# Performance work log

Hardware: AMD Instinct MI355X
Metric: run time of the kernel (lower is better)

## Reference

```python
import jax, jax.numpy as jnp
import numpy as np

NUM_HEADS = 12
WS = 8
ROPE_BASE = 100.0  # croco/dust3r RoPE2D default frequency base


def _rope1d(t, p, inv_freq):
    # t: [Bw, h, N, d], p: [Bw, N], inv_freq: [d/2]
    freqs = p[..., None] * inv_freq                      # [Bw, N, d/2]
    emb = jnp.concatenate([freqs, freqs], axis=-1)       # [Bw, N, d]
    cos = jnp.cos(emb)[:, None, :, :]
    sin = jnp.sin(emb)[:, None, :, :]
    t1, t2 = jnp.split(t, 2, axis=-1)
    rot = jnp.concatenate([-t2, t1], axis=-1)            # rotate_half
    return t * cos + rot * sin


def _rope2d(tokens, pos):
    # tokens: [Bw, h, N, D], pos: [Bw, N, 2] (y, x). First D/2 dims use y, last D/2 use x.
    D = tokens.shape[-1]
    d = D // 2
    inv_freq = 1.0 / (ROPE_BASE ** (jnp.arange(0, d, 2, dtype=jnp.float32) / d))
    ty, tx = jnp.split(tokens, 2, axis=-1)
    return jnp.concatenate([_rope1d(ty, pos[..., 0], inv_freq),
                            _rope1d(tx, pos[..., 1], inv_freq)], axis=-1)


def setup_inputs() -> dict:
    B, H, W, C = 16, 64, 64, 768
    key = jax.random.key(0)
    ks = jax.random.split(key, 7)
    x_img = jax.random.normal(ks[0], (B, H * W, C), dtype=jnp.float32)
    yy, xx = jnp.meshgrid(jnp.arange(H), jnp.arange(W), indexing='ij')
    pos = jnp.stack([yy, xx], axis=-1).reshape(1, H * W, 2).astype(jnp.float32)
    pos2d_img = jnp.broadcast_to(pos, (B, H * W, 2))
    unseen = jax.random.normal(ks[1], (B, C), dtype=jnp.float32)
    sc = C ** -0.5
    qkv_w = jax.random.normal(ks[2], (3 * C, C), dtype=jnp.float32) * sc
    qkv_b = jax.random.normal(ks[3], (3 * C,), dtype=jnp.float32) * 0.02
    proj_w = jax.random.normal(ks[4], (C, C), dtype=jnp.float32) * sc
    proj_b = jax.random.normal(ks[5], (C,), dtype=jnp.float32) * 0.02
    return {'x_img': x_img, 'pos2d_img': pos2d_img, 'unseen': unseen,
            'qkv_w': qkv_w, 'qkv_b': qkv_b, 'proj_w': proj_w, 'proj_b': proj_b,
            'H': H, 'W': W}


def reference(x_img, pos2d_img, unseen, qkv_w, qkv_b, proj_w, proj_b, H, W):
    B, HW, C = x_img.shape
    hd = C // NUM_HEADS
    scale = hd ** -0.5
    nWh, nWw = H // WS, W // WS
    Bwin, Nwin = B * nWh * nWw, WS * WS

    # window partition
    xw = x_img.reshape(B, nWh, WS, nWw, WS, C).transpose(0, 1, 3, 2, 4, 5).reshape(Bwin, Nwin, C)
    pw = pos2d_img.reshape(B, nWh, WS, nWw, WS, 2).transpose(0, 1, 3, 2, 4, 5).reshape(Bwin, Nwin, 2)

    # append unseen token (shared across windows of an image)
    u = jnp.broadcast_to(unseen[:, None, None, :], (B, nWh * nWw, 1, C)).reshape(Bwin, 1, C)
    xw = jnp.concatenate([xw, u], axis=1)                # [Bwin, Nwin+1, C]

    qkv = xw @ qkv_w.T + qkv_b                           # [Bwin, N, 3C]
    qkv = qkv.reshape(Bwin, Nwin + 1, 3, NUM_HEADS, hd)
    q = qkv[:, :, 0].transpose(0, 2, 1, 3)               # [Bwin, h, N, hd]
    k = qkv[:, :, 1].transpose(0, 2, 1, 3)
    v = qkv[:, :, 2].transpose(0, 2, 1, 3)

    # RoPE2D on image tokens only; unseen token gets no RoPE
    q = jnp.concatenate([_rope2d(q[:, :, :Nwin], pw), q[:, :, Nwin:]], axis=2)
    k = jnp.concatenate([_rope2d(k[:, :, :Nwin], pw), k[:, :, Nwin:]], axis=2)

    attn = jax.nn.softmax(jnp.einsum('bhqd,bhkd->bhqk', q, k) * scale, axis=-1)
    out = jnp.einsum('bhqk,bhkd->bhqd', attn, v)
    out = out.transpose(0, 2, 1, 3).reshape(Bwin, Nwin + 1, C)
    out = out @ proj_w.T + proj_b

    # window merge
    out_img = out[:, :Nwin].reshape(B, nWh, nWw, WS, WS, C).transpose(0, 1, 3, 2, 4, 5).reshape(B, HW, C)
    out_unseen = out[:, Nwin].reshape(B, nWh * nWw, C).mean(axis=1)  # [B, C]
    return out_img, out_unseen
```

## Files before the change

kernel.cpp:

```cpp
#include <hip/hip_runtime.h>
#include <cstdint>
#include <cstddef>

typedef __attribute__((ext_vector_type(8)))  __bf16 bf16x8;
typedef __attribute__((ext_vector_type(4)))  float  f32x4;
typedef __attribute__((ext_vector_type(2)))  unsigned int u32x2;

#define DI __device__ __forceinline__

constexpr int Cdim = 768;
constexpr int C3   = 2304;
constexpr int NT   = 65;
constexpr int ROWS = 1024 * NT;
constexpr int ROWS_PAD = ROWS + 32;
constexpr int TP   = 96;
constexpr int PS   = 128;
constexpr long long OUT_IMG = 16LL * 4096 * 768;

DI float bf2f(unsigned short u) { unsigned int x = (unsigned int)u << 16; float f; __builtin_memcpy(&f, &x, 4); return f; }
DI unsigned short f2bf(float f) { unsigned int x; __builtin_memcpy(&x, &f, 4); x = x + 0x7fffu + ((x >> 16) & 1u); return (unsigned short)(x >> 16); }

DI void gload_lds16(const unsigned short* g, unsigned short* l) {
  __builtin_amdgcn_global_load_lds((__attribute__((address_space(1))) void*)g,
                                   (__attribute__((address_space(3))) void*)l, 16, 0, 0);
}

__global__ void k_prep(const float* __restrict__ qkv_w, const float* __restrict__ proj_w,
                       unsigned short* __restrict__ wqb, unsigned short* __restrict__ wpb,
                       float* __restrict__ rope) {
  const int NW1 = 2304 * 768;
  const int NW2 = 768 * 768;
  int total = NW1 + NW2 + 1024;
  for (int i = blockIdx.x * blockDim.x + threadIdx.x; i < total; i += gridDim.x * blockDim.x) {
    if (i < NW1) wqb[i] = f2bf(qkv_w[i]);
    else if (i < NW1 + NW2) wpb[i - NW1] = f2bf(proj_w[i - NW1]);
    else {
      int e = i - NW1 - NW2;
      int p = e >> 4, j = e & 15;
      float inv = powf(100.f, -(float)j * (1.f / 16.f));
      float a = (float)p * inv;
      rope[2 * e]     = cosf(a);
      rope[2 * e + 1] = sinf(a);
    }
  }
}

__global__ void k_xw(const float* __restrict__ x, const float* __restrict__ unseen,
                     unsigned short* __restrict__ xw) {
  int row = blockIdx.x;
  int w = row / NT, t = row - w * NT;
  const float* src;
  if (t == 64) {
    src = unseen + (size_t)(w >> 6) * Cdim;
  } else {
    int wy = (w >> 3) & 7, wx = w & 7;
    int hw = ((wy << 3) + (t >> 3)) * 64 + (wx << 3) + (t & 7);
    src = x + ((size_t)(w >> 6) * 4096 + hw) * Cdim;
  }
  float4 v = ((const float4*)src)[threadIdx.x];
  unsigned int u0 = (unsigned)f2bf(v.x) | ((unsigned)f2bf(v.y) << 16);
  unsigned int u1 = (unsigned)f2bf(v.z) | ((unsigned)f2bf(v.w) << 16);
  ((u32x2*)(xw + (size_t)row * Cdim))[threadIdx.x] = (u32x2){u0, u1};
}

template<int MODE, int NTILES>
__global__ __launch_bounds__(256) void k_gemm(
    const unsigned short* __restrict__ A, const unsigned short* __restrict__ Bw,
    const float* __restrict__ bias, const float* __restrict__ rope,
    unsigned short* __restrict__ Cb, float* __restrict__ outp) {
  constexpr int K = 768;
  __shared__ alignas(16) unsigned short As[128 * 64];
  __shared__ alignas(16) unsigned short Bs[128 * 64];

  constexpr int nwg = 520 * NTILES;
  int id = blockIdx.x;
  int wg = (id & 7) * (nwg >> 3) + (id >> 3);
  int mtile = wg / NTILES, ntile = wg - mtile * NTILES;
  int m0 = mtile * 128, n0 = ntile * 128;

  int tid = threadIdx.x;
  int lane = tid & 63, wid = tid >> 6;
  int lq = lane & 15, lg = lane >> 4;
  int wm = (wid >> 1) * 64, wn = (wid & 1) * 64;

  f32x4 acc[4][4];
  #pragma unroll
  for (int i = 0; i < 4; ++i)
    #pragma unroll
    for (int j = 0; j < 4; ++j) acc[i][j] = (f32x4){0.f, 0.f, 0.f, 0.f};

  for (int kt = 0; kt < K / 64; ++kt) {
    int k0 = kt * 64;
    #pragma unroll
    for (int c = 0; c < 4; ++c) {
      int chunk = c * 256 + tid;
      int row = chunk >> 3, kc = chunk & 7;
      int skc = kc ^ (row & 7);
      gload_lds16(A + (size_t)(m0 + row) * K + k0 + skc * 8,
                  As + (size_t)(c * 256 + (tid & ~63)) * 8);
    }
    #pragma unroll
    for (int c = 0; c < 4; ++c) {
      int chunk = c * 256 + tid;
      int row = chunk >> 3, kc = chunk & 7;
      int skc = kc ^ (row & 7);
      gload_lds16(Bw + (size_t)(n0 + row) * K + k0 + skc * 8,
                  Bs + (size_t)(c * 256 + (tid & ~63)) * 8);
    }
    asm volatile("s_waitcnt vmcnt(0)" ::: "memory");
    __syncthreads();
    #pragma unroll
    for (int ks = 0; ks < 2; ++ks) {
      bf16x8 af[4], bfr[4];
      #pragma unroll
      for (int mt = 0; mt < 4; ++mt) {
        int row = wm + mt * 16 + lq;
        int ch = ((ks << 2) + lg) ^ (row & 7);
        af[mt] = *(const bf16x8*)(As + row * 64 + ch * 8);
      }
      #pragma unroll
      for (int nt = 0; nt < 4; ++nt) {
        int row = wn + nt * 16 + lq;
        int ch = ((ks << 2) + lg) ^ (row & 7);
        bfr[nt] = *(const bf16x8*)(Bs + row * 64 + ch * 8);
      }
      #pragma unroll
      for (int mt = 0; mt < 4; ++mt)
        #pragma unroll
        for (int nt = 0; nt < 4; ++nt)
          acc[mt][nt] = __builtin_amdgcn_mfma_f32_16x16x32_bf16(af[mt], bfr[nt], acc[mt][nt], 0, 0, 0);
    }
    __syncthreads();
  }

  #pragma unroll
  for (int mt = 0; mt < 4; ++mt) {
    #pragma unroll
    for (int r = 0; r < 4; ++r) {
      int row = m0 + wm + mt * 16 + (lg << 2) + r;
      int w = row / NT, t = row - w * NT;
      int wy = (w >> 3) & 7, wx = w & 7;
      int py = (wy << 3) + (t >> 3), px = (wx << 3) + (t & 7);
      #pragma unroll
      for (int a = 0; a < 2; ++a) {
        int col0 = n0 + wn + a * 32 + lq;
        int col1 = col0 + 16;
        float v0 = acc[mt][2 * a][r] + bias[col0];
        float v1 = acc[mt][2 * a + 1][r] + bias[col1];
        if (MODE == 0) {
          if (col0 < 1536 && t != 64) {
            int p = a ? px : py;
            const float* rp = rope + ((p << 4) + lq) * 2;
            float cc = rp[0], ss = rp[1];
            float o0 = v0 * cc - v1 * ss;
            float o1 = v1 * cc + v0 * ss;
            v0 = o0; v1 = o1;
          }
          unsigned short* cr = Cb + (size_t)row * C3;
          cr[col0] = f2bf(v0);
          cr[col1] = f2bf(v1);
        } else {
          if (t == 64) {
            float* ub = outp + OUT_IMG + (size_t)(w >> 6) * Cdim;
            atomicAdd(ub + col0, v0 * (1.f / 64.f));
            atomicAdd(ub + col1, v1 * (1.f / 64.f));
          } else {
            float* orow = outp + ((size_t)(w >> 6) * 4096 + py * 64 + px) * Cdim;
            orow[col0] = v0;
            orow[col1] = v1;
          }
        }
      }
    }
  }
}

__global__ void k_vt(const unsigned short* __restrict__ qkv, unsigned short* __restrict__ Vt) {
  int bh = blockIdx.x;
  int w = bh / 12, h = bh - w * 12;
  __shared__ float sv[65][65];
  const unsigned short* base = qkv + (size_t)w * NT * C3 + 1536 + h * 64;
  for (int i = threadIdx.x; i < 65 * 64; i += 256) {
    int t = i >> 6, d = i & 63;
    sv[t][d] = bf2f(base[(size_t)t * C3 + d]);
  }
  __syncthreads();
  unsigned short* out = Vt + (size_t)bh * 64 * TP;
  for (int i = threadIdx.x; i < 64 * TP; i += 256) {
    int d = i / TP, t = i - d * TP;
    out[i] = f2bf(t < 65 ? sv[t][d] : 0.f);
  }
}

__global__ __launch_bounds__(64) void k_attn(const unsigned short* __restrict__ qkv,
                                             const unsigned short* __restrict__ Vt,
                                             unsigned short* __restrict__ att) {
  __shared__ alignas(16) unsigned short P[80 * PS];
  int h = blockIdx.x, w = blockIdx.y;
  int lane = threadIdx.x;
  int lq = lane & 15, lg = lane >> 4;

  const unsigned short* qb = qkv + (size_t)w * NT * C3 + h * 64;
  const unsigned short* kb = qb + 768;

  bf16x8 kf[5][2];
  #pragma unroll
  for (int kt = 0; kt < 5; ++kt)
    #pragma unroll
    for (int ks = 0; ks < 2; ++ks)
      kf[kt][ks] = *(const bf16x8*)(kb + (size_t)(kt * 16 + lq) * C3 + ks * 32 + lg * 8);

  const unsigned short* vb = Vt + (size_t)(w * 12 + h) * 64 * TP;
  bf16x8 vf[3][4];
  #pragma unroll
  for (int ks = 0; ks < 3; ++ks)
    #pragma unroll
    for (int dt = 0; dt < 4; ++dt)
      vf[ks][dt] = *(const bf16x8*)(vb + (size_t)(dt * 16 + lq) * TP + ks * 32 + lg * 8);

  for (int i = lane; i < 80 * 8; i += 64) {
    int row = i >> 3, j = i & 7;
    int byteo = row * (PS * 2) + 160 + j * 4;
    byteo ^= (row & 7) << 4;
    *(unsigned int*)((char*)P + byteo) = 0u;
  }

  #pragma unroll 1
  for (int qt = 0; qt < 5; ++qt) {
    bf16x8 qf[2];
    #pragma unroll
    for (int ks = 0; ks < 2; ++ks)
      qf[ks] = *(const bf16x8*)(qb + (size_t)(qt * 16 + lq) * C3 + ks * 32 + lg * 8);

    f32x4 sa[5];
    #pragma unroll
    for (int kt = 0; kt < 5; ++kt) {
      sa[kt] = (f32x4){0.f, 0.f, 0.f, 0.f};
      #pragma unroll
      for (int ks = 0; ks < 2; ++ks)
        sa[kt] = __builtin_amdgcn_mfma_f32_16x16x32_bf16(kf[kt][ks], qf[ks], sa[kt], 0, 0, 0);
    }
    float pv[5][4];
    float m = -1e30f;
    #pragma unroll
    for (int kt = 0; kt < 5; ++kt)
      #pragma unroll
      for (int r = 0; r < 4; ++r) {
        int tok = kt * 16 + lg * 4 + r;
        float s = sa[kt][r] * 0.125f;
        bool ok = tok < 65;
        pv[kt][r] = ok ? s : -1e30f;
        m = (ok && s > m) ? s : m;
      }
    m = fmaxf(m, __shfl_xor(m, 16));
    m = fmaxf(m, __shfl_xor(m, 32));
    float sum = 0.f;
    #pragma unroll
    for (int kt = 0; kt < 5; ++kt)
      #pragma unroll
      for (int r = 0; r < 4; ++r) {
        float e = (pv[kt][r] > -1e29f) ? exp2f((pv[kt][r] - m) * 1.44269504f) : 0.f;
        pv[kt][r] = e;
        sum += e;
      }
    sum += __shfl_xor(sum, 16);
    sum += __shfl_xor(sum, 32);
    float rinv = 1.f / sum;

    int q = qt * 16 + lq;
    #pragma unroll
    for (int kt = 0; kt < 5; ++kt) {
      unsigned int u0 = (unsigned)f2bf(pv[kt][0] * rinv) | ((unsigned)f2bf(pv[kt][1] * rinv) << 16);
      unsigned int u1 = (unsigned)f2bf(pv[kt][2] * rinv) | ((unsigned)f2bf(pv[kt][3] * rinv) << 16);
      int byteo = q * (PS * 2) + kt * 32 + lg * 8;
      byteo ^= (q & 7) << 4;
      *(u32x2*)((char*)P + byteo) = (u32x2){u0, u1};
    }
    asm volatile("s_waitcnt lgkmcnt(0)" ::: "memory");

    bf16x8 bp[3];
    #pragma unroll
    for (int ks = 0; ks < 3; ++ks) {
      int byteo = q * (PS * 2) + ks * 64 + lg * 16;
      byteo ^= (q & 7) << 4;
      bp[ks] = *(const bf16x8*)((char*)P + byteo);
    }
    #pragma unroll
    for (int dt = 0; dt < 4; ++dt) {
      f32x4 o = (f32x4){0.f, 0.f, 0.f, 0.f};
      #pragma unroll
      for (int ks = 0; ks < 3; ++ks)
        o = __builtin_amdgcn_mfma_f32_16x16x32_bf16(vf[ks][dt], bp[ks], o, 0, 0, 0);
      if (q < 65) {
        unsigned int u0 = (unsigned)f2bf(o[0]) | ((unsigned)f2bf(o[1]) << 16);
        unsigned int u1 = (unsigned)f2bf(o[2]) | ((unsigned)f2bf(o[3]) << 16);
        *(u32x2*)(att + (size_t)(w * NT + q) * Cdim + h * 64 + dt * 16 + lg * 4) = (u32x2){u0, u1};
      }
    }
  }
}

extern "C" void kernel_launch(void* const* d_in, const int* in_sizes, int n_in,
                              void* d_out, int out_size, void* d_ws, size_t ws_size,
                              hipStream_t stream) {
  const float* x_img  = (const float*)d_in[0];
  const float* unseen = (const float*)d_in[2];
  const float* qkv_w  = (const float*)d_in[3];
  const float* qkv_b  = (const float*)d_in[4];
  const float* proj_w = (const float*)d_in[5];
  const float* proj_b = (const float*)d_in[6];

  char* ws = (char*)d_ws;
  size_t off = 0;
  auto alloc = [&](size_t bytes) { void* p = ws + off; off = (off + bytes + 255) & ~(size_t)255; return p; };
  unsigned short* xw  = (unsigned short*)alloc((size_t)ROWS * Cdim * 2);
  unsigned short* qkv = (unsigned short*)alloc((size_t)ROWS_PAD * C3 * 2);
  unsigned short* Vt  = (unsigned short*)alloc((size_t)12288 * 64 * TP * 2);
  unsigned short* wqb = (unsigned short*)alloc((size_t)C3 * Cdim * 2);
  unsigned short* wpb = (unsigned short*)alloc((size_t)Cdim * Cdim * 2);
  float* rope = (float*)alloc(64 * 16 * 2 * sizeof(float));

  hipMemsetAsync((float*)d_out + OUT_IMG, 0, 16 * Cdim * sizeof(float), stream);

  k_prep<<<512, 256, 0, stream>>>(qkv_w, proj_w, wqb, wpb, rope);
  k_xw<<<ROWS, 192, 0, stream>>>(x_img, unseen, xw);
  k_gemm<0, 18><<<520 * 18, 256, 0, stream>>>(xw, wqb, qkv_b, rope, qkv, nullptr);
  k_vt<<<12288, 256, 0, stream>>>(qkv, Vt);
  k_attn<<<dim3(12, 1024), 64, 0, stream>>>(qkv, Vt, xw);
  k_gemm<1, 6><<<520 * 6, 256, 0, stream>>>(xw, wpb, proj_b, nullptr, nullptr, (float*)d_out);
}
```

Before: 739.7 us.

## Use 256x256 GEMM tiles with a 4-stage LDS prefetch pipeline

Rewrites the shared bf16 GEMM used for the QKV and output projections. Each 512-thread workgroup now computes a 256x256 tile, stepping through K in chunks of 32. Up to three future K-slices are prefetched into a four-buffer LDS ring via direct global-to-LDS loads, with fine-grained vmcnt waits and raised scheduling priority around the MFMA blocks. The aim is to hide global-load latency and raise per-tile data reuse. In exchange, the XOR bank swizzle is dropped, which may cause LDS bank conflicts, and the kernel now uses far more LDS and accumulator registers per workgroup.

```diff
diff --git a/kernel.cpp b/kernel.cpp
--- a/kernel.cpp
+++ b/kernel.cpp
@@ -64,80 +64,107 @@
 }
 
 template<int MODE, int NTILES>
-__global__ __launch_bounds__(256) void k_gemm(
+__global__ __launch_bounds__(512, 2) void k_gemm(
     const unsigned short* __restrict__ A, const unsigned short* __restrict__ Bw,
     const float* __restrict__ bias, const float* __restrict__ rope,
     unsigned short* __restrict__ Cb, float* __restrict__ outp) {
   constexpr int K = 768;
-  __shared__ alignas(16) unsigned short As[128 * 64];
-  __shared__ alignas(16) unsigned short Bs[128 * 64];
-
-  constexpr int nwg = 520 * NTILES;
+  constexpr int NK = K / 32;
+  constexpr int BUF = 16384;
+  __shared__ alignas(16) unsigned short lds[4 * BUF];
+
+  constexpr int nwg = 260 * NTILES;
+  constexpr int q8 = nwg / 8, r8 = nwg % 8;
   int id = blockIdx.x;
-  int wg = (id & 7) * (nwg >> 3) + (id >> 3);
+  int xcd = id & 7, lid = id >> 3;
+  int wg = (xcd < r8 ? xcd * (q8 + 1) : r8 * (q8 + 1) + (xcd - r8) * q8) + lid;
   int mtile = wg / NTILES, ntile = wg - mtile * NTILES;
-  int m0 = mtile * 128, n0 = ntile * 128;
+  int m0 = mtile * 256, n0 = ntile * 256;
 
   int tid = threadIdx.x;
   int lane = tid & 63, wid = tid >> 6;
   int lq = lane & 15, lg = lane >> 4;
-  int wm = (wid >> 1) * 64, wn = (wid & 1) * 64;
-
-  f32x4 acc[4][4];
+  int wm = (wid >> 2) * 128;
+  int wn = (wid & 3) * 64;
+
+  auto stageA = [&](int tt) {
+    unsigned short* d = lds + (tt & 3) * BUF;
+    int k0 = tt * 32;
+    #pragma unroll
+    for (int c = 0; c < 2; ++c) {
+      int chunk = c * 512 + tid;
+      gload_lds16(A + (size_t)(m0 + (chunk >> 2)) * K + k0 + (chunk & 3) * 8,
+                  d + (size_t)(c * 512 + (tid & ~63)) * 8);
+    }
+  };
+  auto stageB = [&](int tt) {
+    unsigned short* d = lds + (tt & 3) * BUF + 8192;
+    int k0 = tt * 32;
+    #pragma unroll
+    for (int c = 0; c < 2; ++c) {
+      int chunk = c * 512 + tid;
+      gload_lds16(Bw + (size_t)(n0 + (chunk >> 2)) * K + k0 + (chunk & 3) * 8,
+                  d + (size_t)(c * 512 + (tid & ~63)) * 8);
+    }
+  };
+
+  f32x4 acc[8][4];
   #pragma unroll
-  for (int i = 0; i < 4; ++i)
+  for (int i = 0; i < 8; ++i)
     #pragma unroll
     for (int j = 0; j < 4; ++j) acc[i][j] = (f32x4){0.f, 0.f, 0.f, 0.f};
 
-  for (int kt = 0; kt < K / 64; ++kt) {
-    int k0 = kt * 64;
-    #pragma unroll
-    for (int c = 0; c < 4; ++c) {
-      int chunk = c * 256 + tid;
-      int row = chunk >> 3, kc = chunk & 7;
-      int skc = kc ^ (row & 7);
-      gload_lds16(A + (size_t)(m0 + row) * K + k0 + skc * 8,
-                  As + (size_t)(c * 256 + (tid & ~63)) * 8);
-    }
-    #pragma unroll
-    for (int c = 0; c < 4; ++c) {
-      int chunk = c * 256 + tid;
-      int row = chunk >> 3, kc = chunk & 7;
-      int skc = kc ^ (row & 7);
-      gload_lds16(Bw + (size_t)(n0 + row) * K + k0 + skc * 8,
-                  Bs + (size_t)(c * 256 + (tid & ~63)) * 8);
-    }
-    asm volatile("s_waitcnt vmcnt(0)" ::: "memory");
-    __syncthreads();
-    #pragma unroll
-    for (int ks = 0; ks < 2; ++ks) {
-      bf16x8 af[4], bfr[4];
-      #pragma unroll
-      for (int mt = 0; mt < 4; ++mt) {
-        int row = wm + mt * 16 + lq;
-        int ch = ((ks << 2) + lg) ^ (row & 7);
-        af[mt] = *(const bf16x8*)(As + row * 64 + ch * 8);
-      }
-      #pragma unroll
-      for (int nt = 0; nt < 4; ++nt) {
-        int row = wn + nt * 16 + lq;
-        int ch = ((ks << 2) + lg) ^ (row & 7);
-        bfr[nt] = *(const bf16x8*)(Bs + row * 64 + ch * 8);
-      }
-      #pragma unroll
-      for (int mt = 0; mt < 4; ++mt)
-        #pragma unroll
-        for (int nt = 0; nt < 4; ++nt)
-          acc[mt][nt] = __builtin_amdgcn_mfma_f32_16x16x32_bf16(af[mt], bfr[nt], acc[mt][nt], 0, 0, 0);
-    }
-    __syncthreads();
+  stageA(0); stageB(0);
+  stageA(1); stageB(1);
+  stageA(2); stageB(2);
+  asm volatile("s_waitcnt vmcnt(8)\n\ts_barrier" ::: "memory");
+
+  for (int t = 0; t < NK; ++t) {
+    const unsigned short* sA = lds + (t & 3) * BUF;
+    const unsigned short* sB = sA + 8192;
+    int tp = t + 3;
+
+    bf16x8 bfr[4], af[4];
+    #pragma unroll
+    for (int nf = 0; nf < 4; ++nf)
+      bfr[nf] = *(const bf16x8*)(sB + (wn + nf * 16 + lq) * 32 + lg * 8);
+    #pragma unroll
+    for (int mf = 0; mf < 4; ++mf)
+      af[mf] = *(const bf16x8*)(sA + (wm + mf * 16 + lq) * 32 + lg * 8);
+    if (tp < NK) stageA(tp);
+    __builtin_amdgcn_s_setprio(1);
+    #pragma unroll
+    for (int mf = 0; mf < 4; ++mf)
+      #pragma unroll
+      for (int nf = 0; nf < 4; ++nf)
+        acc[mf][nf] = __builtin_amdgcn_mfma_f32_16x16x32_bf16(af[mf], bfr[nf], acc[mf][nf], 0, 0, 0);
+    __builtin_amdgcn_s_setprio(0);
+
+    bf16x8 af2[4];
+    #pragma unroll
+    for (int mf = 0; mf < 4; ++mf)
+      af2[mf] = *(const bf16x8*)(sA + (wm + 64 + mf * 16 + lq) * 32 + lg * 8);
+    if (tp < NK) stageB(tp);
+    __builtin_amdgcn_s_setprio(1);
+    #pragma unroll
+    for (int mf = 0; mf < 4; ++mf)
+      #pragma unroll
+      for (int nf = 0; nf < 4; ++nf)
+        acc[4 + mf][nf] = __builtin_amdgcn_mfma_f32_16x16x32_bf16(af2[mf], bfr[nf], acc[4 + mf][nf], 0, 0, 0);
+    __builtin_amdgcn_s_setprio(0);
+
+    if (t < NK - 1) {
+      if (t <= NK - 4)      asm volatile("s_waitcnt vmcnt(8)\n\ts_barrier" ::: "memory");
+      else if (t == NK - 3) asm volatile("s_waitcnt vmcnt(4)\n\ts_barrier" ::: "memory");
+      else                  asm volatile("s_waitcnt vmcnt(0)\n\ts_barrier" ::: "memory");
+    }
   }
 
   #pragma unroll
-  for (int mt = 0; mt < 4; ++mt) {
+  for (int mf = 0; mf < 8; ++mf) {
     #pragma unroll
     for (int r = 0; r < 4; ++r) {
-      int row = m0 + wm + mt * 16 + (lg << 2) + r;
+      int row = m0 + wm + mf * 16 + (lg << 2) + r;
       int w = row / NT, t = row - w * NT;
       int wy = (w >> 3) & 7, wx = w & 7;
       int py = (wy << 3) + (t >> 3), px = (wx << 3) + (t & 7);
@@ -145,8 +172,8 @@
       for (int a = 0; a < 2; ++a) {
         int col0 = n0 + wn + a * 32 + lq;
         int col1 = col0 + 16;
-        float v0 = acc[mt][2 * a][r] + bias[col0];
-        float v1 = acc[mt][2 * a + 1][r] + bias[col1];
+        float v0 = acc[mf][2 * a][r] + bias[col0];
+        float v1 = acc[mf][2 * a + 1][r] + bias[col1];
         if (MODE == 0) {
           if (col0 < 1536 && t != 64) {
             int p = a ? px : py;
@@ -324,8 +351,8 @@
 
   k_prep<<<512, 256, 0, stream>>>(qkv_w, proj_w, wqb, wpb, rope);
   k_xw<<<ROWS, 192, 0, stream>>>(x_img, unseen, xw);
-  k_gemm<0, 18><<<520 * 18, 256, 0, stream>>>(xw, wqb, qkv_b, rope, qkv, nullptr);
+  k_gemm<0, 9><<<260 * 9, 512, 0, stream>>>(xw, wqb, qkv_b, rope, qkv, nullptr);
   k_vt<<<12288, 256, 0, stream>>>(qkv, Vt);
   k_attn<<<dim3(12, 1024), 64, 0, stream>>>(qkv, Vt, xw);
-  k_gemm<1, 6><<<520 * 6, 256, 0, stream>>>(xw, wpb, proj_b, nullptr, nullptr, (float*)d_out);
-}
+  k_gemm<1, 3><<<260 * 3, 512, 0, stream>>>(xw, wpb, proj_b, nullptr, nullptr, (float*)d_out);
+}
```

Result: faster. 686.2 us (-7.2%).

## Enlarge GEMM M tile to 256 rows with 128x64 per-wave tiles

Applied to the files above, without the earlier changes.

The GEMM tile grows from 128x128 to 256x128, and each wave now computes a 128x64 sub-tile with 32 accumulators. B fragments are loaded once per k-step and reused across two halves of A fragments, which halves the number of workgroups and the redundant B traffic. The XCD remap is generalised for block counts not divisible by 8, and the explicit vmcnt wait is removed. This raises register and LDS pressure (launch_bounds 256,2) and reduces the number of blocks in flight, which risks lower occupancy and less latency hiding.

```diff
diff --git a/kernel.cpp b/kernel.cpp
--- a/kernel.cpp
+++ b/kernel.cpp
@@ -64,80 +64,90 @@
 }
 
 template<int MODE, int NTILES>
-__global__ __launch_bounds__(256) void k_gemm(
+__global__ __launch_bounds__(256, 2) void k_gemm(
     const unsigned short* __restrict__ A, const unsigned short* __restrict__ Bw,
     const float* __restrict__ bias, const float* __restrict__ rope,
     unsigned short* __restrict__ Cb, float* __restrict__ outp) {
   constexpr int K = 768;
-  __shared__ alignas(16) unsigned short As[128 * 64];
+  constexpr int NK = K / 64;
+  __shared__ alignas(16) unsigned short As[256 * 64];
   __shared__ alignas(16) unsigned short Bs[128 * 64];
 
-  constexpr int nwg = 520 * NTILES;
+  constexpr int nwg = 260 * NTILES;
+  constexpr int q8 = nwg / 8, r8 = nwg % 8;
   int id = blockIdx.x;
-  int wg = (id & 7) * (nwg >> 3) + (id >> 3);
+  int xcd = id & 7, lid = id >> 3;
+  int wg = (xcd < r8 ? xcd * (q8 + 1) : r8 * (q8 + 1) + (xcd - r8) * q8) + lid;
   int mtile = wg / NTILES, ntile = wg - mtile * NTILES;
-  int m0 = mtile * 128, n0 = ntile * 128;
+  int m0 = mtile * 256, n0 = ntile * 128;
 
   int tid = threadIdx.x;
   int lane = tid & 63, wid = tid >> 6;
   int lq = lane & 15, lg = lane >> 4;
-  int wm = (wid >> 1) * 64, wn = (wid & 1) * 64;
-
-  f32x4 acc[4][4];
+  int wm = (wid >> 1) * 128;
+  int wn = (wid & 1) * 64;
+
+  f32x4 acc[8][4];
   #pragma unroll
-  for (int i = 0; i < 4; ++i)
+  for (int i = 0; i < 8; ++i)
     #pragma unroll
     for (int j = 0; j < 4; ++j) acc[i][j] = (f32x4){0.f, 0.f, 0.f, 0.f};
 
-  for (int kt = 0; kt < K / 64; ++kt) {
+  #pragma unroll 1
+  for (int kt = 0; kt < NK; ++kt) {
     int k0 = kt * 64;
     #pragma unroll
-    for (int c = 0; c < 4; ++c) {
-      int chunk = c * 256 + tid;
-      int row = chunk >> 3, kc = chunk & 7;
-      int skc = kc ^ (row & 7);
-      gload_lds16(A + (size_t)(m0 + row) * K + k0 + skc * 8,
-                  As + (size_t)(c * 256 + (tid & ~63)) * 8);
-    }
-    #pragma unroll
-    for (int c = 0; c < 4; ++c) {
-      int chunk = c * 256 + tid;
-      int row = chunk >> 3, kc = chunk & 7;
-      int skc = kc ^ (row & 7);
-      gload_lds16(Bw + (size_t)(n0 + row) * K + k0 + skc * 8,
-                  Bs + (size_t)(c * 256 + (tid & ~63)) * 8);
-    }
-    asm volatile("s_waitcnt vmcnt(0)" ::: "memory");
+    for (int j = 0; j < 8; ++j) {
+      int slot = j * 256 + tid;
+      int row = slot >> 3, c = slot & 7;
+      gload_lds16(A + (size_t)(m0 + row) * K + k0 + (c ^ (row & 7)) * 8,
+                  As + (size_t)(j * 256 + (tid & ~63)) * 8);
+    }
+    #pragma unroll
+    for (int j = 0; j < 4; ++j) {
+      int slot = j * 256 + tid;
+      int row = slot >> 3, c = slot & 7;
+      gload_lds16(Bw + (size_t)(n0 + row) * K + k0 + (c ^ (row & 7)) * 8,
+                  Bs + (size_t)(j * 256 + (tid & ~63)) * 8);
+    }
     __syncthreads();
-    #pragma unroll
-    for (int ks = 0; ks < 2; ++ks) {
-      bf16x8 af[4], bfr[4];
-      #pragma unroll
-      for (int mt = 0; mt < 4; ++mt) {
-        int row = wm + mt * 16 + lq;
-        int ch = ((ks << 2) + lg) ^ (row & 7);
-        af[mt] = *(const bf16x8*)(As + row * 64 + ch * 8);
-      }
-      #pragma unroll
-      for (int nt = 0; nt < 4; ++nt) {
-        int row = wn + nt * 16 + lq;
-        int ch = ((ks << 2) + lg) ^ (row & 7);
-        bfr[nt] = *(const bf16x8*)(Bs + row * 64 + ch * 8);
-      }
-      #pragma unroll
-      for (int mt = 0; mt < 4; ++mt)
+
+    bf16x8 bfr[8];
+    #pragma unroll
+    for (int nf = 0; nf < 4; ++nf)
+      #pragma unroll
+      for (int ks = 0; ks < 2; ++ks) {
+        int row = wn + nf * 16 + lq;
+        bfr[nf * 2 + ks] = *(const bf16x8*)(Bs + row * 64 + (((ks * 4 + lg) ^ (row & 7)) * 8));
+      }
+    #pragma unroll
+    for (int half = 0; half < 2; ++half) {
+      bf16x8 af[8];
+      #pragma unroll
+      for (int mf = 0; mf < 4; ++mf)
         #pragma unroll
-        for (int nt = 0; nt < 4; ++nt)
-          acc[mt][nt] = __builtin_amdgcn_mfma_f32_16x16x32_bf16(af[mt], bfr[nt], acc[mt][nt], 0, 0, 0);
+        for (int ks = 0; ks < 2; ++ks) {
+          int row = wm + half * 64 + mf * 16 + lq;
+          af[mf * 2 + ks] = *(const bf16x8*)(As + row * 64 + (((ks * 4 + lg) ^ (row & 7)) * 8));
+        }
+      #pragma unroll
+      for (int mf = 0; mf < 4; ++mf)
+        #pragma unroll
+        for (int nf = 0; nf < 4; ++nf)
+          #pragma unroll
+          for (int ks = 0; ks < 2; ++ks)
+            acc[half * 4 + mf][nf] =
+              __builtin_amdgcn_mfma_f32_16x16x32_bf16(af[mf * 2 + ks], bfr[nf * 2 + ks],
+                                                      acc[half * 4 + mf][nf], 0, 0, 0);
     }
     __syncthreads();
   }
 
   #pragma unroll
-  for (int mt = 0; mt < 4; ++mt) {
+  for (int mf = 0; mf < 8; ++mf) {
     #pragma unroll
     for (int r = 0; r < 4; ++r) {
-      int row = m0 + wm + mt * 16 + (lg << 2) + r;
+      int row = m0 + wm + mf * 16 + (lg << 2) + r;
       int w = row / NT, t = row - w * NT;
       int wy = (w >> 3) & 7, wx = w & 7;
       int py = (wy << 3) + (t >> 3), px = (wx << 3) + (t & 7);
@@ -145,8 +155,8 @@
       for (int a = 0; a < 2; ++a) {
         int col0 = n0 + wn + a * 32 + lq;
         int col1 = col0 + 16;
-        float v0 = acc[mt][2 * a][r] + bias[col0];
-        float v1 = acc[mt][2 * a + 1][r] + bias[col1];
+        float v0 = acc[mf][2 * a][r] + bias[col0];
+        float v1 = acc[mf][2 * a + 1][r] + bias[col1];
         if (MODE == 0) {
           if (col0 < 1536 && t != 64) {
             int p = a ? px : py;
@@ -324,8 +334,8 @@
 
   k_prep<<<512, 256, 0, stream>>>(qkv_w, proj_w, wqb, wpb, rope);
   k_xw<<<ROWS, 192, 0, stream>>>(x_img, unseen, xw);
-  k_gemm<0, 18><<<520 * 18, 256, 0, stream>>>(xw, wqb, qkv_b, rope, qkv, nullptr);
+  k_gemm<0, 18><<<260 * 18, 256, 0, stream>>>(xw, wqb, qkv_b, rope, qkv, nullptr);
   k_vt<<<12288, 256, 0, stream>>>(qkv, Vt);
   k_attn<<<dim3(12, 1024), 64, 0, stream>>>(qkv, Vt, xw);
-  k_gemm<1, 6><<<520 * 6, 256, 0, stream>>>(xw, wpb, proj_b, nullptr, nullptr, (float*)d_out);
-}
+  k_gemm<1, 6><<<260 * 6, 256, 0, stream>>>(xw, wpb, proj_b, nullptr, nullptr, (float*)d_out);
+}
```

Measured after the change: 725.3 us. No clear change (-2.0%).

## Stage GEMM epilogues through swizzled LDS for coalesced 16-byte global stores

Applied to the files above, without the earlier changes.

The GEMM epilogues now write results into shared memory using an XOR swizzle, then store to global memory with coalesced 128-bit writes. This replaces the old scattered 2-byte and 4-byte stores, in both the QKV (bf16) and projection (fp32, done in two halves) paths. The Vt transpose kernel now packs eight bf16 values per 16-byte store, the workgroup-to-XCD remap handles counts not divisible by 8, and launch bounds request 4 waves per SIMD. The tradeoff is extra LDS round trips and barriers in the epilogue, plus possible register pressure from the occupancy hint.

```diff
diff --git a/kernel.cpp b/kernel.cpp
--- a/kernel.cpp
+++ b/kernel.cpp
@@ -5,6 +5,7 @@
 typedef __attribute__((ext_vector_type(8)))  __bf16 bf16x8;
 typedef __attribute__((ext_vector_type(4)))  float  f32x4;
 typedef __attribute__((ext_vector_type(2)))  unsigned int u32x2;
+typedef __attribute__((ext_vector_type(4)))  unsigned int u32x4;
 
 #define DI __device__ __forceinline__
 
@@ -64,7 +65,7 @@
 }
 
 template<int MODE, int NTILES>
-__global__ __launch_bounds__(256) void k_gemm(
+__global__ __launch_bounds__(256, 4) void k_gemm(
     const unsigned short* __restrict__ A, const unsigned short* __restrict__ Bw,
     const float* __restrict__ bias, const float* __restrict__ rope,
     unsigned short* __restrict__ Cb, float* __restrict__ outp) {
@@ -73,15 +74,18 @@
   __shared__ alignas(16) unsigned short Bs[128 * 64];
 
   constexpr int nwg = 520 * NTILES;
+  constexpr int q8 = nwg / 8, r8 = nwg % 8;
   int id = blockIdx.x;
-  int wg = (id & 7) * (nwg >> 3) + (id >> 3);
+  int xcd = id & 7, lid = id >> 3;
+  int wg = (xcd < r8 ? xcd * (q8 + 1) : r8 * (q8 + 1) + (xcd - r8) * q8) + lid;
   int mtile = wg / NTILES, ntile = wg - mtile * NTILES;
   int m0 = mtile * 128, n0 = ntile * 128;
 
   int tid = threadIdx.x;
   int lane = tid & 63, wid = tid >> 6;
   int lq = lane & 15, lg = lane >> 4;
-  int wm = (wid >> 1) * 64, wn = (wid & 1) * 64;
+  int wm = (wid >> 1) * 64;
+  int wn = (wid & 1) * 64;
 
   f32x4 acc[4][4];
   #pragma unroll
@@ -133,21 +137,23 @@
     __syncthreads();
   }
 
-  #pragma unroll
-  for (int mt = 0; mt < 4; ++mt) {
-    #pragma unroll
-    for (int r = 0; r < 4; ++r) {
-      int row = m0 + wm + mt * 16 + (lg << 2) + r;
-      int w = row / NT, t = row - w * NT;
-      int wy = (w >> 3) & 7, wx = w & 7;
-      int py = (wy << 3) + (t >> 3), px = (wx << 3) + (t & 7);
-      #pragma unroll
-      for (int a = 0; a < 2; ++a) {
-        int col0 = n0 + wn + a * 32 + lq;
-        int col1 = col0 + 16;
-        float v0 = acc[mt][2 * a][r] + bias[col0];
-        float v1 = acc[mt][2 * a + 1][r] + bias[col1];
-        if (MODE == 0) {
+  if (MODE == 0) {
+    unsigned short* ct = As;
+    #pragma unroll
+    for (int mt = 0; mt < 4; ++mt) {
+      #pragma unroll
+      for (int r = 0; r < 4; ++r) {
+        int lrow = wm + mt * 16 + (lg << 2) + r;
+        int grow = m0 + lrow;
+        int w = grow / NT, t = grow - w * NT;
+        int wy = (w >> 3) & 7, wx = w & 7;
+        int py = (wy << 3) + (t >> 3), px = (wx << 3) + (t & 7);
+        #pragma unroll
+        for (int a = 0; a < 2; ++a) {
+          int cn0 = wn + a * 32 + lq;
+          int col0 = n0 + cn0, col1 = col0 + 16;
+          float v0 = acc[mt][2 * a][r] + bias[col0];
+          float v1 = acc[mt][2 * a + 1][r] + bias[col1];
           if (col0 < 1536 && t != 64) {
             int p = a ? px : py;
             const float* rp = rope + ((p << 4) + lq) * 2;
@@ -156,21 +162,68 @@
             float o1 = v1 * cc + v0 * ss;
             v0 = o0; v1 = o1;
           }
-          unsigned short* cr = Cb + (size_t)row * C3;
-          cr[col0] = f2bf(v0);
-          cr[col1] = f2bf(v1);
-        } else {
-          if (t == 64) {
-            float* ub = outp + OUT_IMG + (size_t)(w >> 6) * Cdim;
-            atomicAdd(ub + col0, v0 * (1.f / 64.f));
-            atomicAdd(ub + col1, v1 * (1.f / 64.f));
-          } else {
-            float* orow = outp + ((size_t)(w >> 6) * 4096 + py * 64 + px) * Cdim;
-            orow[col0] = v0;
-            orow[col1] = v1;
+          int b0 = (lrow * 256 + cn0 * 2) ^ ((lrow & 7) << 4);
+          int b1 = (lrow * 256 + (cn0 + 16) * 2) ^ ((lrow & 7) << 4);
+          *(unsigned short*)((char*)ct + b0) = f2bf(v0);
+          *(unsigned short*)((char*)ct + b1) = f2bf(v1);
+        }
+      }
+    }
+    __syncthreads();
+    #pragma unroll
+    for (int j = 0; j < 8; ++j) {
+      int idx = j * 256 + tid;
+      int row = idx >> 4, c = idx & 15;
+      u32x4 v = *(const u32x4*)((char*)ct + row * 256 + ((c ^ (row & 7)) << 4));
+      *(u32x4*)(Cb + (size_t)(m0 + row) * C3 + n0 + c * 8) = v;
+    }
+  } else {
+    float* cf = (float*)As;
+    #pragma unroll
+    for (int half = 0; half < 2; ++half) {
+      if ((wm >> 6) == half) {
+        #pragma unroll
+        for (int mt = 0; mt < 4; ++mt) {
+          #pragma unroll
+          for (int r = 0; r < 4; ++r) {
+            int lrow = mt * 16 + (lg << 2) + r;
+            int grow = m0 + half * 64 + lrow;
+            int w = grow / NT, t = grow - w * NT;
+            #pragma unroll
+            for (int a = 0; a < 2; ++a) {
+              int cn0 = wn + a * 32 + lq;
+              int col0 = n0 + cn0, col1 = col0 + 16;
+              float v0 = acc[mt][2 * a][r] + bias[col0];
+              float v1 = acc[mt][2 * a + 1][r] + bias[col1];
+              if (t == 64) {
+                float* ub = outp + OUT_IMG + (size_t)(w >> 6) * Cdim;
+                atomicAdd(ub + col0, v0 * (1.f / 64.f));
+                atomicAdd(ub + col1, v1 * (1.f / 64.f));
+              } else {
+                int b0 = (lrow * 512 + cn0 * 4) ^ ((lrow & 7) << 4);
+                int b1 = (lrow * 512 + (cn0 + 16) * 4) ^ ((lrow & 7) << 4);
+                *(float*)((char*)cf + b0) = v0;
+                *(float*)((char*)cf + b1) = v1;
+              }
+            }
           }
         }
       }
+      __syncthreads();
+      #pragma unroll
+      for (int j = 0; j < 8; ++j) {
+        int idx = j * 256 + tid;
+        int row = idx >> 5, c = idx & 31;
+        int grow = m0 + half * 64 + row;
+        int w = grow / NT, t = grow - w * NT;
+        if (t != 64) {
+          int wy = (w >> 3) & 7, wx = w & 7;
+          int py = (wy << 3) + (t >> 3), px = (wx << 3) + (t & 7);
+          u32x4 v = *(const u32x4*)((char*)cf + row * 512 + ((c ^ (row & 7)) << 4));
+          *(u32x4*)(outp + ((size_t)(w >> 6) * 4096 + py * 64 + px) * Cdim + n0 + c * 4) = v;
+        }
+      }
+      __syncthreads();
     }
   }
 }
@@ -186,9 +239,18 @@
   }
   __syncthreads();
   unsigned short* out = Vt + (size_t)bh * 64 * TP;
-  for (int i = threadIdx.x; i < 64 * TP; i += 256) {
-    int d = i / TP, t = i - d * TP;
-    out[i] = f2bf(t < 65 ? sv[t][d] : 0.f);
+  for (int i = threadIdx.x; i < 64 * (TP / 8); i += 256) {
+    int d = i / (TP / 8), tc = i - d * (TP / 8);
+    int t0 = tc * 8;
+    unsigned int u[4];
+    #pragma unroll
+    for (int k = 0; k < 4; ++k) {
+      int ta = t0 + 2 * k, tb = ta + 1;
+      unsigned short sa = (ta < 65) ? f2bf(sv[ta][d]) : (unsigned short)0;
+      unsigned short sb = (tb < 65) ? f2bf(sv[tb][d]) : (unsigned short)0;
+      u[k] = (unsigned)sa | ((unsigned)sb << 16);
+    }
+    *(u32x4*)(out + d * TP + t0) = (u32x4){u[0], u[1], u[2], u[3]};
   }
 }
 
```

Measured after the change: 658.0 us. 1.12x faster.
